# Performance work log

Hardware: AMD Instinct MI355X
Metric: run time of the kernel (lower is better)

## Reference

```python
import jax, jax.numpy as jnp
import numpy as np


def setup_inputs() -> dict:
    key = jax.random.key(0)
    ks = jax.random.split(key, 10)
    B, S, C, H, NC, T = 128, 512, 512, 512, 64, 25
    s = 0.02  # init scale
    return {
        "x": jax.random.normal(ks[0], (B, S, C), jnp.float32),
        "text": jax.random.randint(ks[1], (B, T + 1), 0, NC),
        "W_i2h": jax.random.normal(ks[2], (C, H), jnp.float32) * s,
        "W_h2h": jax.random.normal(ks[3], (H, H), jnp.float32) * s,
        "b_h2h": jnp.zeros((H,), jnp.float32),
        "W_score": jax.random.normal(ks[4], (H, 1), jnp.float32) * s,
        "W_lstm": jax.random.normal(ks[5], (C + NC, 4 * H), jnp.float32) * s,
        "U_lstm": jax.random.normal(ks[6], (H, 4 * H), jnp.float32) * s,
        "b_lstm": jnp.zeros((4 * H,), jnp.float32),
        "W_gen": jax.random.normal(ks[7], (H, NC), jnp.float32) * s,
        "b_gen": jnp.zeros((NC,), jnp.float32),
        "batch_max_length": 25,
    }


def reference(x, text, W_i2h, W_h2h, b_h2h, W_score, W_lstm, U_lstm, b_lstm,
              W_gen, b_gen, batch_max_length):
    B = x.shape[0]
    H = W_h2h.shape[0]
    NC = W_gen.shape[1]
    T = batch_max_length

    # i2h(batch_H) is loop-invariant -> compute once. [B,S,H]
    batch_H_proj = jnp.einsum('bsc,ch->bsh', x, W_i2h)
    # one-hot teacher-forcing inputs, time-major for scan. [T,B,NC]
    onehots_t = jnp.swapaxes(jax.nn.one_hot(text[:, :T], NC, dtype=x.dtype), 0, 1)

    def step(carry, char_oh):
        h, c = carry
        hp = (h @ W_h2h + b_h2h)[:, None, :]                 # [B,1,H]
        e = jnp.tanh(batch_H_proj + hp) @ W_score            # [B,S,1]
        alpha = jax.nn.softmax(e, axis=1)                    # [B,S,1]
        context = jnp.einsum('bs,bsc->bc', alpha[..., 0], x) # [B,C]
        inp = jnp.concatenate([context, char_oh], axis=1)    # [B,C+NC]
        # Keras LSTMCell gate math: z split into i,f,g,o chunks
        z = inp @ W_lstm + h @ U_lstm + b_lstm               # [B,4H]
        zi, zf, zg, zo = jnp.split(z, 4, axis=1)
        i = jax.nn.sigmoid(zi)
        f = jax.nn.sigmoid(zf)
        g = jnp.tanh(zg)
        o = jax.nn.sigmoid(zo)
        c_new = f * c + i * g
        h_new = o * jnp.tanh(c_new)
        return (h_new, c_new), h_new

    init = (jnp.zeros((B, H), x.dtype), jnp.zeros((B, H), x.dtype))
    _, hs = jax.lax.scan(step, init, onehots_t)              # [T,B,H]
    output_hiddens = jnp.swapaxes(hs, 0, 1)                  # [B,T,H]
    probs = output_hiddens @ W_gen + b_gen                   # [B,T,NC]
    return probs
```

## Files before the change

kernel.cpp:

```cpp
#include <hip/hip_runtime.h>
#include <hip/hip_bf16.h>

#define B_ 128
#define S_ 512
#define C_ 512
#define H_ 512
#define NC_ 64
#define T_ 25
#define TEXTW (T_ + 1)

typedef __attribute__((ext_vector_type(8))) short bf16x8;
typedef __attribute__((ext_vector_type(8))) unsigned short u16x8;
typedef __attribute__((ext_vector_type(4))) float f32x4;

__device__ __forceinline__ float bf2f(unsigned short u) {
    union { unsigned int i; float f; } v; v.i = ((unsigned int)u) << 16; return v.f;
}
__device__ __forceinline__ unsigned short f2bf(float f) {
    union { float f; unsigned int u; } v; v.f = f;
    unsigned int r = (v.u + 0x7FFFu + ((v.u >> 16) & 1u)) >> 16;
    return (unsigned short)r;
}
__device__ __forceinline__ void gload_lds16(const void* g, void* l) {
    __builtin_amdgcn_global_load_lds(
        (const __attribute__((address_space(1))) unsigned int*)g,
        (__attribute__((address_space(3))) unsigned int*)l, 16, 0, 0);
}
__device__ __forceinline__ float fast_tanh(float x) {
    float e = __builtin_amdgcn_exp2f(2.885390082f * x);
    return 1.f - 2.f * __builtin_amdgcn_rcpf(e + 1.f);
}
__device__ __forceinline__ float fast_sigmoid(float x) {
    return __builtin_amdgcn_rcpf(1.f + __builtin_amdgcn_exp2f(-1.442695041f * x));
}

__global__ __launch_bounds__(512) void setup_k(
    const float* __restrict__ Wi, const float* __restrict__ Wh,
    const float* __restrict__ Wl, const float* __restrict__ Ul,
    unsigned short* __restrict__ Wt_bf, unsigned short* __restrict__ Wh_bf,
    unsigned short* __restrict__ WU_t,
    float* __restrict__ c2, unsigned short* __restrict__ inp) {
    int blk = blockIdx.x, tid = threadIdx.x;
    if (blk < 128) {
        c2[blk * 512 + tid] = 0.f;
        c2[65536 + blk * 512 + tid] = 0.f;
        inp[blk * 1024 + 512 + tid] = 0;
    } else if (blk < 640) {
        int n = blk - 128;
        Wt_bf[n * 512 + tid] = f2bf(Wi[tid * 512 + n]);
    } else if (blk < 1152) {
        int i = (blk - 640) * 512 + tid;
        Wh_bf[i] = f2bf(Wh[i]);
    } else {
        int np = blk - 1152;
        int h = np >> 2, g = np & 3;
        {
            float v = Wl[(size_t)tid * 2048 + g * 512 + h];
            WU_t[(size_t)np * 1024 + tid] = f2bf(v);
        }
        {
            float v = Ul[(size_t)tid * 2048 + g * 512 + h];
            WU_t[(size_t)np * 1024 + 512 + tid] = f2bf(v);
        }
    }
}

__global__ __launch_bounds__(256) void conv_x(const float* __restrict__ in,
                                              unsigned short* __restrict__ out) {
    int i = blockIdx.x * 256 + threadIdx.x;
    const float4 v = ((const float4*)in)[i];
    ushort4 o;
    o.x = f2bf(v.x); o.y = f2bf(v.y); o.z = f2bf(v.z); o.w = f2bf(v.w);
    ((ushort4*)out)[i] = o;
}

__global__ __launch_bounds__(256) void gemm_proj(const unsigned short* __restrict__ A,
                                                 const unsigned short* __restrict__ Bt,
                                                 unsigned short* __restrict__ Cm) {
    __shared__ unsigned short As[128 * 64];
    __shared__ unsigned short Bs[128 * 64];
    int tid = threadIdx.x;
    int lane = tid & 63;
    int wid = tid >> 6;
    int wr = wid >> 1, wc = wid & 1;
    int row0 = blockIdx.y * 128;
    int col0 = blockIdx.x * 128;

    f32x4 acc[4][4];
#pragma unroll
    for (int i = 0; i < 4; ++i)
#pragma unroll
        for (int j = 0; j < 4; ++j) acc[i][j] = (f32x4){0.f, 0.f, 0.f, 0.f};

    for (int k0 = 0; k0 < 512; k0 += 64) {
#pragma unroll
        for (int i = 0; i < 4; ++i) {
            int e = tid + i * 256;
            int r = e >> 3, cc = e & 7;
            int cs = cc ^ (r & 7);
            gload_lds16(A + (size_t)(row0 + r) * 512 + k0 + cs * 8, &As[e * 8]);
        }
#pragma unroll
        for (int i = 0; i < 4; ++i) {
            int e = tid + i * 256;
            int r = e >> 3, cc = e & 7;
            int cs = cc ^ (r & 7);
            gload_lds16(Bt + (size_t)(col0 + r) * 512 + k0 + cs * 8, &Bs[e * 8]);
        }
        __syncthreads();
#pragma unroll
        for (int ks = 0; ks < 2; ++ks) {
            bf16x8 a[4], b[4];
#pragma unroll
            for (int i = 0; i < 4; ++i) {
                int m = wr * 64 + i * 16 + (lane & 15);
                int ch = (ks * 4 + (lane >> 4)) ^ (m & 7);
                a[i] = *(const bf16x8*)&As[(m * 8 + ch) * 8];
            }
#pragma unroll
            for (int j = 0; j < 4; ++j) {
                int n = wc * 64 + j * 16 + (lane & 15);
                int ch = (ks * 4 + (lane >> 4)) ^ (n & 7);
                b[j] = *(const bf16x8*)&Bs[(n * 8 + ch) * 8];
            }
#pragma unroll
            for (int i = 0; i < 4; ++i)
#pragma unroll
                for (int j = 0; j < 4; ++j)
                    acc[i][j] = __builtin_amdgcn_mfma_f32_16x16x32_bf16(a[i], b[j], acc[i][j], 0, 0, 0);
        }
        __syncthreads();
    }
#pragma unroll
    for (int i = 0; i < 4; ++i)
#pragma unroll
        for (int j = 0; j < 4; ++j) {
            int gcol = col0 + wc * 64 + j * 16 + (lane & 15);
#pragma unroll
            for (int r = 0; r < 4; ++r) {
                int grow = row0 + wr * 64 + i * 16 + (lane >> 4) * 4 + r;
                Cm[(size_t)grow * 512 + gcol] = f2bf(acc[i][j][r]);
            }
        }
}

__global__ __launch_bounds__(512) void z_gemm(
    const unsigned short* __restrict__ inp, const unsigned short* __restrict__ Bt,
    const float* __restrict__ pc, const float* __restrict__ pm,
    const float* __restrict__ ps, float* __restrict__ Z) {
    __shared__ unsigned short As[8192];
    __shared__ unsigned short Bs[4096];
    int tid = threadIdx.x;
    int lane = tid & 63;
    int wave = tid >> 6;
    int wr = wave >> 2, wc = wave & 3;
    int col0 = blockIdx.x * 64;

    float cw0[2], cw1[2];
    int rr[2], csv[2];
#pragma unroll
    for (int i = 0; i < 2; ++i) {
        int e = tid + i * 512;
        int r = e >> 3, cc = e & 7;
        rr[i] = r; csv[i] = cc ^ (r & 7);
        float m0 = pm[r], m1 = pm[128 + r];
        float s0 = ps[r], s1 = ps[128 + r];
        float M = fmaxf(m0, m1);
        float w0 = __builtin_amdgcn_exp2f(1.442695041f * (m0 - M));
        float w1 = __builtin_amdgcn_exp2f(1.442695041f * (m1 - M));
        float inv = 1.f / (w0 * s0 + w1 * s1);
        cw0[i] = w0 * inv; cw1[i] = w1 * inv;
    }

    f32x4 acc[4];
#pragma unroll
    for (int i = 0; i < 4; ++i) acc[i] = (f32x4){0.f, 0.f, 0.f, 0.f};

    for (int k0 = 0; k0 < 1024; k0 += 64) {
        if (k0 < 512) {
#pragma unroll
            for (int i = 0; i < 2; ++i) {
                int e = tid + i * 512;
                int kb = k0 + csv[i] * 8;
                const float* c0p = pc + rr[i] * 512 + kb;
                const float* c1p = pc + 65536 + rr[i] * 512 + kb;
                float4 c0a = *(const float4*)c0p;
                float4 c0b = *(const float4*)(c0p + 4);
                float4 c1a = *(const float4*)c1p;
                float4 c1b = *(const float4*)(c1p + 4);
                u16x8 o;
                o[0] = f2bf(cw0[i] * c0a.x + cw1[i] * c1a.x);
                o[1] = f2bf(cw0[i] * c0a.y + cw1[i] * c1a.y);
                o[2] = f2bf(cw0[i] * c0a.z + cw1[i] * c1a.z);
                o[3] = f2bf(cw0[i] * c0a.w + cw1[i] * c1a.w);
                o[4] = f2bf(cw0[i] * c0b.x + cw1[i] * c1b.x);
                o[5] = f2bf(cw0[i] * c0b.y + cw1[i] * c1b.y);
                o[6] = f2bf(cw0[i] * c0b.z + cw1[i] * c1b.z);
                o[7] = f2bf(cw0[i] * c0b.w + cw1[i] * c1b.w);
                *(u16x8*)&As[e * 8] = o;
            }
        } else {
#pragma unroll
            for (int i = 0; i < 2; ++i) {
                int e = tid + i * 512;
                gload_lds16(inp + (size_t)rr[i] * 1024 + k0 + csv[i] * 8, &As[e * 8]);
            }
        }
        {
            int e = tid;
            int r = e >> 3, cc = e & 7;
            int cs = cc ^ (r & 7);
            gload_lds16(Bt + (size_t)(col0 + r) * 1024 + k0 + cs * 8, &Bs[e * 8]);
        }
        __syncthreads();
#pragma unroll
        for (int ks = 0; ks < 2; ++ks) {
            bf16x8 a[4], bfr;
#pragma unroll
            for (int i = 0; i < 4; ++i) {
                int m = wr * 64 + i * 16 + (lane & 15);
                int ch = (ks * 4 + (lane >> 4)) ^ (m & 7);
                a[i] = *(const bf16x8*)&As[(m * 8 + ch) * 8];
            }
            {
                int n = wc * 16 + (lane & 15);
                int ch = (ks * 4 + (lane >> 4)) ^ (n & 7);
                bfr = *(const bf16x8*)&Bs[(n * 8 + ch) * 8];
            }
#pragma unroll
            for (int i = 0; i < 4; ++i)
                acc[i] = __builtin_amdgcn_mfma_f32_16x16x32_bf16(a[i], bfr, acc[i], 0, 0, 0);
        }
        __syncthreads();
    }
#pragma unroll
    for (int i = 0; i < 4; ++i) {
        int gcol = col0 + wc * 16 + (lane & 15);
#pragma unroll
        for (int r = 0; r < 4; ++r) {
            int grow = wr * 64 + i * 16 + (lane >> 4) * 4 + r;
            Z[(size_t)grow * 2048 + gcol] = acc[i][r];
        }
    }
}

__global__ __launch_bounds__(1024) void ghp_e2(
    const float* __restrict__ z, const int* __restrict__ text,
    const float* __restrict__ Wl, const float* __restrict__ bl,
    const unsigned short* __restrict__ Whb, const float* __restrict__ bh2h,
    float* __restrict__ c2, float* __restrict__ hs_t,
    unsigned short* __restrict__ inp,
    const unsigned short* __restrict__ proj, const unsigned short* __restrict__ xb,
    const float* __restrict__ Wscore,
    float* __restrict__ pc, float* __restrict__ pm, float* __restrict__ ps, int t) {
    __shared__ float shg[512];
    __shared__ float gp[16][512];
    __shared__ float sh_hp[512];
    __shared__ float sh_e[256];
    __shared__ float sh_alpha[256];
    __shared__ float sh_red[8];
    __shared__ float shp[8][512];
    int blk = blockIdx.x;
    int half = blk >> 7, b = blk & 127;
    int tid = threadIdx.x, wave = tid >> 6, lane = tid & 63;

    if (t >= 0) {
        if (tid < 512) {
            int ch = text[b * TEXTW + t];
            const float* wrow = Wl + (size_t)(512 + ch) * 2048;
            float4 zv = *(const float4*)(z + (size_t)b * 2048 + tid * 4);
            float zi = zv.x + bl[tid] + wrow[tid];
            float zf = zv.y + bl[512 + tid] + wrow[512 + tid];
            float zg = zv.z + bl[1024 + tid] + wrow[1024 + tid];
            float zo = zv.w + bl[1536 + tid] + wrow[1536 + tid];
            float ig = fast_sigmoid(zi);
            float fg = fast_sigmoid(zf);
            float gg = fast_tanh(zg);
            float og = fast_sigmoid(zo);
            int idx = half * 65536 + b * 512 + tid;
            float cn = fg * c2[idx] + ig * gg;
            c2[idx] = cn;
            float hn = og * fast_tanh(cn);
            if (half == 0) {
                hs_t[b * 512 + tid] = hn;
                inp[b * 1024 + 512 + tid] = f2bf(hn);
            }
            shg[tid] = hn;
        }
        __syncthreads();
        if (t >= T_ - 1) return;
        {
            float r8[8] = {0.f, 0.f, 0.f, 0.f, 0.f, 0.f, 0.f, 0.f};
#pragma unroll 4
            for (int kk = 0; kk < 32; ++kk) {
                int k = wave * 32 + kk;
                float hv = shg[k];
                u16x8 wv = *(const u16x8*)(Whb + k * 512 + lane * 8);
#pragma unroll
                for (int jj = 0; jj < 8; ++jj) r8[jj] = fmaf(hv, bf2f(wv[jj]), r8[jj]);
            }
#pragma unroll
            for (int jj = 0; jj < 8; ++jj) gp[wave][lane * 8 + jj] = r8[jj];
        }
        __syncthreads();
        if (tid < 512) {
            float s = bh2h[tid];
#pragma unroll
            for (int w = 0; w < 16; ++w) s += gp[w][tid];
            sh_hp[tid] = s;
        }
        __syncthreads();
    } else {
        if (tid < 512) sh_hp[tid] = bh2h[tid];
        __syncthreads();
    }

    {
        float4 h0 = *(const float4*)(sh_hp + lane * 8);
        float4 h1 = *(const float4*)(sh_hp + lane * 8 + 4);
        float4 w0 = *(const float4*)(Wscore + lane * 8);
        float4 w1 = *(const float4*)(Wscore + lane * 8 + 4);
        float hp_r[8] = {h0.x, h0.y, h0.z, h0.w, h1.x, h1.y, h1.z, h1.w};
        float w_r[8]  = {w0.x, w0.y, w0.z, w0.w, w1.x, w1.y, w1.z, w1.w};
        float w2_r[8];
#pragma unroll
        for (int j = 0; j < 8; ++j) w2_r[j] = -2.f * w_r[j];
        int s0g = half * 256 + wave * 16;
        for (int i = 0; i < 16; i += 4) {
            bf16x8 pv[4];
#pragma unroll
            for (int q = 0; q < 4; ++q)
                pv[q] = *(const bf16x8*)(proj + ((size_t)(b * 512 + s0g + i + q) << 9) + lane * 8);
#pragma unroll
            for (int q = 0; q < 4; ++q) {
                float a = 0.f;
#pragma unroll
                for (int j = 0; j < 8; ++j) {
                    float xv = bf2f((unsigned short)pv[q][j]) + hp_r[j];
                    float r = __builtin_amdgcn_rcpf(__builtin_amdgcn_exp2f(2.885390082f * xv) + 1.f);
                    a += w_r[j];
                    a = fmaf(w2_r[j], r, a);
                }
#pragma unroll
                for (int off = 32; off > 0; off >>= 1) a += __shfl_xor(a, off, 64);
                if (lane == 0) sh_e[wave * 16 + i + q] = a;
            }
        }
    }
    __syncthreads();

    if (tid < 256) {
        float v = sh_e[tid];
        float m = v;
#pragma unroll
        for (int off = 32; off > 0; off >>= 1) m = fmaxf(m, __shfl_xor(m, off, 64));
        if (lane == 0) sh_red[wave] = m;
    }
    __syncthreads();
    if (tid < 256) {
        float mh = fmaxf(fmaxf(sh_red[0], sh_red[1]), fmaxf(sh_red[2], sh_red[3]));
        float p = __builtin_amdgcn_exp2f(1.442695041f * (sh_e[tid] - mh));
        float ss = p;
#pragma unroll
        for (int off = 32; off > 0; off >>= 1) ss += __shfl_xor(ss, off, 64);
        if (lane == 0) sh_red[4 + wave] = ss;
        sh_alpha[tid] = p;
    }
    __syncthreads();
    if (tid == 0) {
        pm[half * 128 + b] = fmaxf(fmaxf(sh_red[0], sh_red[1]), fmaxf(sh_red[2], sh_red[3]));
        ps[half * 128 + b] = sh_red[4] + sh_red[5] + sh_red[6] + sh_red[7];
    }

    {
        int cc = wave >> 3, sg = wave & 7;
        int col = cc * 256 + lane * 4;
        float a0 = 0.f, a1 = 0.f, a2 = 0.f, a3 = 0.f;
#pragma unroll 4
        for (int sl = sg; sl < 256; sl += 8) {
            float al = sh_alpha[sl];
            int s = half * 256 + sl;
            ushort4 xv = *(const ushort4*)(xb + ((size_t)(b * 512 + s) << 9) + col);
            a0 = fmaf(al, bf2f(xv.x), a0);
            a1 = fmaf(al, bf2f(xv.y), a1);
            a2 = fmaf(al, bf2f(xv.z), a2);
            a3 = fmaf(al, bf2f(xv.w), a3);
        }
        *(float4*)&shp[sg][col] = make_float4(a0, a1, a2, a3);
    }
    __syncthreads();
    if (tid < 512) {
        float s = 0.f;
#pragma unroll
        for (int r = 0; r < 8; ++r) s += shp[r][tid];
        pc[(size_t)(half * 128 + b) * 512 + tid] = s;
    }
}

__global__ __launch_bounds__(64) void gen_probs(const float* __restrict__ hs,
                                                const float* __restrict__ Wg,
                                                const float* __restrict__ bg,
                                                float* __restrict__ out) {
    __shared__ float sh[512];
    int bt = blockIdx.x;
    int b = bt / T_, t = bt % T_;
    int tid = threadIdx.x;
    const float* hrow = hs + ((size_t)t * B_ + b) * H_;
    for (int i = tid; i < 512; i += 64) sh[i] = hrow[i];
    __syncthreads();
    float acc = bg[tid];
#pragma unroll 4
    for (int k = 0; k < 512; ++k) acc = fmaf(sh[k], Wg[k * 64 + tid], acc);
    out[(size_t)bt * 64 + tid] = acc;
}

extern "C" void kernel_launch(void* const* d_in, const int* in_sizes, int n_in,
                              void* d_out, int out_size, void* d_ws, size_t ws_size,
                              hipStream_t stream) {
    const float* x       = (const float*)d_in[0];
    const int*   text    = (const int*)d_in[1];
    const float* W_i2h   = (const float*)d_in[2];
    const float* W_h2h   = (const float*)d_in[3];
    const float* b_h2h   = (const float*)d_in[4];
    const float* W_score = (const float*)d_in[5];
    const float* W_lstm  = (const float*)d_in[6];
    const float* U_lstm  = (const float*)d_in[7];
    const float* b_lstm  = (const float*)d_in[8];
    const float* W_gen   = (const float*)d_in[9];
    const float* b_gen   = (const float*)d_in[10];
    float* out = (float*)d_out;

    char* ws = (char*)d_ws;
    unsigned short* x_bf    = (unsigned short*)ws;
    unsigned short* proj_bf = (unsigned short*)(ws + 67108864);
    unsigned short* Wt_bf   = (unsigned short*)(ws + 134217728);
    unsigned short* Wh_bf   = (unsigned short*)(ws + 134742016);
    unsigned short* WU_t    = (unsigned short*)(ws + 135266304);
    float* c2      = (float*)(ws + 139460608);
    unsigned short* inp_bf = (unsigned short*)(ws + 139984896);
    float* z_buf   = (float*)(ws + 140247040);
    float* pc      = (float*)(ws + 141295616);
    float* pm      = (float*)(ws + 141819904);
    float* ps      = (float*)(ws + 141820928);
    float* hs      = (float*)(ws + 141821952);

    setup_k<<<dim3(3200), 512, 0, stream>>>(W_i2h, W_h2h, W_lstm, U_lstm,
                                            Wt_bf, Wh_bf, WU_t, c2, inp_bf);
    conv_x<<<dim3(32768), 256, 0, stream>>>(x, x_bf);
    gemm_proj<<<dim3(4, 512), 256, 0, stream>>>(x_bf, Wt_bf, proj_bf);
    ghp_e2<<<dim3(256), 1024, 0, stream>>>(z_buf, text, W_lstm, b_lstm, Wh_bf, b_h2h,
                                           c2, hs, inp_bf, proj_bf, x_bf, W_score,
                                           pc, pm, ps, -1);
    for (int t = 0; t < T_; ++t) {
        z_gemm<<<dim3(32), 512, 0, stream>>>(inp_bf, WU_t, pc, pm, ps, z_buf);
        ghp_e2<<<dim3(256), 1024, 0, stream>>>(z_buf, text, W_lstm, b_lstm, Wh_bf, b_h2h,
                                               c2, hs + (size_t)t * (B_ * H_),
                                               inp_bf, proj_bf, x_bf, W_score,
                                               pc, pm, ps, t);
    }
    gen_probs<<<dim3(B_ * T_), 64, 0, stream>>>(hs, W_gen, b_gen, out);
}
```

Before: 1.468 ms.

## Fuse LSTM gate update and split h2h projection into the z GEMM kernel

Moves the LSTM cell update and a partial h@W_h2h product into the z GEMM kernel. Each of the 32 blocks owns 16 hidden units across all batches, so the z buffer round trip goes away and the update is no longer computed redundantly by two halves. The h2h projection becomes 32 per-block partial sums that the attention kernel reduces, and h is double-buffered. This adds a 32-way partial-sum buffer read from global memory, and only 32 blocks now run the LSTM and h2h work.

```diff
diff --git a/kernel.cpp b/kernel.cpp
--- a/kernel.cpp
+++ b/kernel.cpp
@@ -39,12 +39,11 @@
     const float* __restrict__ Wl, const float* __restrict__ Ul,
     unsigned short* __restrict__ Wt_bf, unsigned short* __restrict__ Wh_bf,
     unsigned short* __restrict__ WU_t,
-    float* __restrict__ c2, unsigned short* __restrict__ inp) {
+    float* __restrict__ c, unsigned short* __restrict__ hb0) {
     int blk = blockIdx.x, tid = threadIdx.x;
     if (blk < 128) {
-        c2[blk * 512 + tid] = 0.f;
-        c2[65536 + blk * 512 + tid] = 0.f;
-        inp[blk * 1024 + 512 + tid] = 0;
+        c[blk * 512 + tid] = 0.f;
+        hb0[blk * 512 + tid] = 0;
     } else if (blk < 640) {
         int n = blk - 128;
         Wt_bf[n * 512 + tid] = f2bf(Wi[tid * 512 + n]);
@@ -144,17 +143,34 @@
         }
 }
 
-__global__ __launch_bounds__(512) void z_gemm(
-    const unsigned short* __restrict__ inp, const unsigned short* __restrict__ Bt,
+__global__ __launch_bounds__(512) void zg_kernel(
+    const unsigned short* __restrict__ hb_cur, const unsigned short* __restrict__ Bt,
     const float* __restrict__ pc, const float* __restrict__ pm,
-    const float* __restrict__ ps, float* __restrict__ Z) {
-    __shared__ unsigned short As[8192];
-    __shared__ unsigned short Bs[4096];
+    const float* __restrict__ ps, const unsigned short* __restrict__ Whb,
+    const int* __restrict__ text, const float* __restrict__ Wl,
+    const float* __restrict__ bl,
+    float* __restrict__ c, float* __restrict__ hs_t,
+    unsigned short* __restrict__ hb_nxt, float* __restrict__ hp_part, int t) {
+    __shared__ union {
+        struct { unsigned short As[8192]; unsigned short Bs[4096]; } s;
+        float zt[128][66];
+    } u;
+    __shared__ float hl_sh[128][16];
+    __shared__ unsigned short wh_sh[16][512];
     int tid = threadIdx.x;
     int lane = tid & 63;
     int wave = tid >> 6;
     int wr = wave >> 2, wc = wave & 3;
     int col0 = blockIdx.x * 64;
+    int h0 = blockIdx.x * 16;
+
+    {
+        int k = tid >> 5, j = (tid & 31) * 16;
+        u16x8 w0 = *(const u16x8*)(Whb + (size_t)(h0 + k) * 512 + j);
+        u16x8 w1 = *(const u16x8*)(Whb + (size_t)(h0 + k) * 512 + j + 8);
+        *(u16x8*)&wh_sh[k][j] = w0;
+        *(u16x8*)&wh_sh[k][j + 8] = w1;
+    }
 
     float cw0[2], cw1[2];
     int rr[2], csv[2];
@@ -197,20 +213,20 @@
                 o[5] = f2bf(cw0[i] * c0b.y + cw1[i] * c1b.y);
                 o[6] = f2bf(cw0[i] * c0b.z + cw1[i] * c1b.z);
                 o[7] = f2bf(cw0[i] * c0b.w + cw1[i] * c1b.w);
-                *(u16x8*)&As[e * 8] = o;
+                *(u16x8*)&u.s.As[e * 8] = o;
             }
         } else {
 #pragma unroll
             for (int i = 0; i < 2; ++i) {
                 int e = tid + i * 512;
-                gload_lds16(inp + (size_t)rr[i] * 1024 + k0 + csv[i] * 8, &As[e * 8]);
+                gload_lds16(hb_cur + (size_t)rr[i] * 512 + (k0 - 512) + csv[i] * 8, &u.s.As[e * 8]);
             }
         }
         {
             int e = tid;
             int r = e >> 3, cc = e & 7;
             int cs = cc ^ (r & 7);
-            gload_lds16(Bt + (size_t)(col0 + r) * 1024 + k0 + cs * 8, &Bs[e * 8]);
+            gload_lds16(Bt + (size_t)(col0 + r) * 1024 + k0 + cs * 8, &u.s.Bs[e * 8]);
         }
         __syncthreads();
 #pragma unroll
@@ -220,12 +236,12 @@
             for (int i = 0; i < 4; ++i) {
                 int m = wr * 64 + i * 16 + (lane & 15);
                 int ch = (ks * 4 + (lane >> 4)) ^ (m & 7);
-                a[i] = *(const bf16x8*)&As[(m * 8 + ch) * 8];
+                a[i] = *(const bf16x8*)&u.s.As[(m * 8 + ch) * 8];
             }
             {
                 int n = wc * 16 + (lane & 15);
                 int ch = (ks * 4 + (lane >> 4)) ^ (n & 7);
-                bfr = *(const bf16x8*)&Bs[(n * 8 + ch) * 8];
+                bfr = *(const bf16x8*)&u.s.Bs[(n * 8 + ch) * 8];
             }
 #pragma unroll
             for (int i = 0; i < 4; ++i)
@@ -233,28 +249,72 @@
         }
         __syncthreads();
     }
+
 #pragma unroll
     for (int i = 0; i < 4; ++i) {
-        int gcol = col0 + wc * 16 + (lane & 15);
-#pragma unroll
-        for (int r = 0; r < 4; ++r) {
-            int grow = wr * 64 + i * 16 + (lane >> 4) * 4 + r;
-            Z[(size_t)grow * 2048 + gcol] = acc[i][r];
-        }
-    }
-}
-
-__global__ __launch_bounds__(1024) void ghp_e2(
-    const float* __restrict__ z, const int* __restrict__ text,
-    const float* __restrict__ Wl, const float* __restrict__ bl,
-    const unsigned short* __restrict__ Whb, const float* __restrict__ bh2h,
-    float* __restrict__ c2, float* __restrict__ hs_t,
-    unsigned short* __restrict__ inp,
+        int gcolL = wc * 16 + (lane & 15);
+#pragma unroll
+        for (int r = 0; r < 4; ++r)
+            u.zt[wr * 64 + i * 16 + (lane >> 4) * 4 + r][gcolL] = acc[i][r];
+    }
+    __syncthreads();
+
+#pragma unroll
+    for (int it = 0; it < 4; ++it) {
+        int item = tid + it * 512;
+        int b = item >> 4, hl = item & 15;
+        int hg = h0 + hl;
+        int ch = text[b * TEXTW + t];
+        const float* wrow = Wl + (size_t)(512 + ch) * 2048;
+        float zi = u.zt[b][hl * 4 + 0] + bl[hg] + wrow[hg];
+        float zf = u.zt[b][hl * 4 + 1] + bl[512 + hg] + wrow[512 + hg];
+        float zgv = u.zt[b][hl * 4 + 2] + bl[1024 + hg] + wrow[1024 + hg];
+        float zo = u.zt[b][hl * 4 + 3] + bl[1536 + hg] + wrow[1536 + hg];
+        float ig = fast_sigmoid(zi);
+        float fg = fast_sigmoid(zf);
+        float gg = fast_tanh(zgv);
+        float og = fast_sigmoid(zo);
+        int idx = b * 512 + hg;
+        float cn = fg * c[idx] + ig * gg;
+        c[idx] = cn;
+        float hn = og * fast_tanh(cn);
+        hs_t[idx] = hn;
+        hb_nxt[idx] = f2bf(hn);
+        hl_sh[b][hl] = hn;
+    }
+    __syncthreads();
+
+    {
+        int j0 = lane * 8;
+        for (int bb = 0; bb < 16; ++bb) {
+            int b = wave * 16 + bb;
+            float a0 = 0.f, a1 = 0.f, a2 = 0.f, a3 = 0.f;
+            float a4 = 0.f, a5 = 0.f, a6 = 0.f, a7 = 0.f;
+#pragma unroll
+            for (int k = 0; k < 16; ++k) {
+                float hv = hl_sh[b][k];
+                u16x8 wv = *(const u16x8*)&wh_sh[k][j0];
+                a0 = fmaf(hv, bf2f(wv[0]), a0);
+                a1 = fmaf(hv, bf2f(wv[1]), a1);
+                a2 = fmaf(hv, bf2f(wv[2]), a2);
+                a3 = fmaf(hv, bf2f(wv[3]), a3);
+                a4 = fmaf(hv, bf2f(wv[4]), a4);
+                a5 = fmaf(hv, bf2f(wv[5]), a5);
+                a6 = fmaf(hv, bf2f(wv[6]), a6);
+                a7 = fmaf(hv, bf2f(wv[7]), a7);
+            }
+            float* dst = hp_part + ((size_t)blockIdx.x * 128 + b) * 512 + j0;
+            *(float4*)dst = make_float4(a0, a1, a2, a3);
+            *(float4*)(dst + 4) = make_float4(a4, a5, a6, a7);
+        }
+    }
+}
+
+__global__ __launch_bounds__(1024) void ehp_kernel(
+    const float* __restrict__ hp_part, const float* __restrict__ bh2h,
     const unsigned short* __restrict__ proj, const unsigned short* __restrict__ xb,
     const float* __restrict__ Wscore,
     float* __restrict__ pc, float* __restrict__ pm, float* __restrict__ ps, int t) {
-    __shared__ float shg[512];
-    __shared__ float gp[16][512];
     __shared__ float sh_hp[512];
     __shared__ float sh_e[256];
     __shared__ float sh_alpha[256];
@@ -264,56 +324,16 @@
     int half = blk >> 7, b = blk & 127;
     int tid = threadIdx.x, wave = tid >> 6, lane = tid & 63;
 
-    if (t >= 0) {
-        if (tid < 512) {
-            int ch = text[b * TEXTW + t];
-            const float* wrow = Wl + (size_t)(512 + ch) * 2048;
-            float4 zv = *(const float4*)(z + (size_t)b * 2048 + tid * 4);
-            float zi = zv.x + bl[tid] + wrow[tid];
-            float zf = zv.y + bl[512 + tid] + wrow[512 + tid];
-            float zg = zv.z + bl[1024 + tid] + wrow[1024 + tid];
-            float zo = zv.w + bl[1536 + tid] + wrow[1536 + tid];
-            float ig = fast_sigmoid(zi);
-            float fg = fast_sigmoid(zf);
-            float gg = fast_tanh(zg);
-            float og = fast_sigmoid(zo);
-            int idx = half * 65536 + b * 512 + tid;
-            float cn = fg * c2[idx] + ig * gg;
-            c2[idx] = cn;
-            float hn = og * fast_tanh(cn);
-            if (half == 0) {
-                hs_t[b * 512 + tid] = hn;
-                inp[b * 1024 + 512 + tid] = f2bf(hn);
-            }
-            shg[tid] = hn;
-        }
-        __syncthreads();
-        if (t >= T_ - 1) return;
-        {
-            float r8[8] = {0.f, 0.f, 0.f, 0.f, 0.f, 0.f, 0.f, 0.f};
-#pragma unroll 4
-            for (int kk = 0; kk < 32; ++kk) {
-                int k = wave * 32 + kk;
-                float hv = shg[k];
-                u16x8 wv = *(const u16x8*)(Whb + k * 512 + lane * 8);
-#pragma unroll
-                for (int jj = 0; jj < 8; ++jj) r8[jj] = fmaf(hv, bf2f(wv[jj]), r8[jj]);
-            }
-#pragma unroll
-            for (int jj = 0; jj < 8; ++jj) gp[wave][lane * 8 + jj] = r8[jj];
-        }
-        __syncthreads();
-        if (tid < 512) {
-            float s = bh2h[tid];
-#pragma unroll
-            for (int w = 0; w < 16; ++w) s += gp[w][tid];
-            sh_hp[tid] = s;
-        }
-        __syncthreads();
-    } else {
-        if (tid < 512) sh_hp[tid] = bh2h[tid];
-        __syncthreads();
-    }
+    if (tid < 512) {
+        float s = bh2h[tid];
+        if (t >= 0) {
+            const float* p = hp_part + b * 512 + tid;
+#pragma unroll 8
+            for (int q = 0; q < 32; ++q) s += p[(size_t)q * 65536];
+        }
+        sh_hp[tid] = s;
+    }
+    __syncthreads();
 
     {
         float4 h0 = *(const float4*)(sh_hp + lane * 8);
@@ -436,27 +456,31 @@
     unsigned short* Wt_bf   = (unsigned short*)(ws + 134217728);
     unsigned short* Wh_bf   = (unsigned short*)(ws + 134742016);
     unsigned short* WU_t    = (unsigned short*)(ws + 135266304);
-    float* c2      = (float*)(ws + 139460608);
-    unsigned short* inp_bf = (unsigned short*)(ws + 139984896);
-    float* z_buf   = (float*)(ws + 140247040);
-    float* pc      = (float*)(ws + 141295616);
-    float* pm      = (float*)(ws + 141819904);
-    float* ps      = (float*)(ws + 141820928);
-    float* hs      = (float*)(ws + 141821952);
+    float* c_buf   = (float*)(ws + 139460608);
+    unsigned short* hb0 = (unsigned short*)(ws + 139722752);
+    unsigned short* hb1 = (unsigned short*)(ws + 139853824);
+    float* pc      = (float*)(ws + 139984896);
+    float* pm      = (float*)(ws + 140509184);
+    float* ps      = (float*)(ws + 140510208);
+    float* hp_part = (float*)(ws + 140511232);
+    float* hs      = (float*)(ws + 148899840);
+
+    unsigned short* hb[2] = {hb0, hb1};
 
     setup_k<<<dim3(3200), 512, 0, stream>>>(W_i2h, W_h2h, W_lstm, U_lstm,
-                                            Wt_bf, Wh_bf, WU_t, c2, inp_bf);
+                                            Wt_bf, Wh_bf, WU_t, c_buf, hb0);
     conv_x<<<dim3(32768), 256, 0, stream>>>(x, x_bf);
     gemm_proj<<<dim3(4, 512), 256, 0, stream>>>(x_bf, Wt_bf, proj_bf);
-    ghp_e2<<<dim3(256), 1024, 0, stream>>>(z_buf, text, W_lstm, b_lstm, Wh_bf, b_h2h,
-                                           c2, hs, inp_bf, proj_bf, x_bf, W_score,
-                                           pc, pm, ps, -1);
+    ehp_kernel<<<dim3(256), 1024, 0, stream>>>(hp_part, b_h2h, proj_bf, x_bf, W_score,
+                                               pc, pm, ps, -1);
     for (int t = 0; t < T_; ++t) {
-        z_gemm<<<dim3(32), 512, 0, stream>>>(inp_bf, WU_t, pc, pm, ps, z_buf);
-        ghp_e2<<<dim3(256), 1024, 0, stream>>>(z_buf, text, W_lstm, b_lstm, Wh_bf, b_h2h,
-                                               c2, hs + (size_t)t * (B_ * H_),
-                                               inp_bf, proj_bf, x_bf, W_score,
-                                               pc, pm, ps, t);
+        zg_kernel<<<dim3(32), 512, 0, stream>>>(hb[t & 1], WU_t, pc, pm, ps, Wh_bf,
+                                                text, W_lstm, b_lstm, c_buf,
+                                                hs + (size_t)t * (B_ * H_),
+                                                hb[(t + 1) & 1], hp_part, t);
+        if (t < T_ - 1)
+            ehp_kernel<<<dim3(256), 1024, 0, stream>>>(hp_part, b_h2h, proj_bf, x_bf, W_score,
+                                                       pc, pm, ps, t);
     }
     gen_probs<<<dim3(B_ * T_), 64, 0, stream>>>(hs, W_gen, b_gen, out);
 }
```

Result: slower. 3.490 ms (+137.6%).
